# Performance work log

Hardware: AMD Instinct MI355X
Metric: run time of the kernel (lower is better)

The kernel has to match this reference:

```python
import jax, jax.numpy as jnp
import numpy as np

BS, N_AGGR, D, OUT = 4096, 4, 128, 128  # d_in per child; T is (A, D+1, D+1, OUT)


def setup_inputs() -> dict:
    key = jax.random.key(0)
    k0, k1, k2 = jax.random.split(key, 3)
    x0 = jax.random.normal(k0, (BS, N_AGGR, D), dtype=jnp.float32)
    x1 = jax.random.normal(k1, (BS, N_AGGR, D), dtype=jnp.float32)
    # xavier-uniform-style init for each T_j, stacked over the aggregator axis
    fan_in = (D + 1) * (D + 1) * OUT // (D + 1)  # torch fan heuristic scale; exact init not load-bearing
    bound = float(np.sqrt(6.0 / ((D + 1) + (D + 1) * OUT)))
    T = jax.random.uniform(k2, (N_AGGR, D + 1, D + 1, OUT), dtype=jnp.float32,
                           minval=-bound, maxval=bound)
    return {"x0": x0, "x1": x1, "T": T}


def reference(x0, x1, T):
    # x0, x1: (bs, A, D); T: (A, D+1, D+1, OUT)
    bs, A, _ = x0.shape
    ones = jnp.ones((bs, A, 1), dtype=x0.dtype)
    h0 = jnp.concatenate([x0, ones], axis=2)            # (bs, A, D+1)
    # first contraction (the per-head matmul loop, fused): (bs, A, D+1, OUT)
    r = jnp.einsum('bai,aijo->bajo', h0, T)
    h1 = jnp.concatenate([x1, ones], axis=2)            # (bs, A, D+1)
    # second contraction (the per-head bmm loop, fused): (bs, A, OUT)
    out = jnp.einsum('baj,bajo->bao', h1, r)
    return out
```

## Files before the change

kernel.cpp:

```cpp
#include <hip/hip_runtime.h>
#include <stdint.h>
#include <stddef.h>

#define NA     4
#define DDIM   128
#define OUTD   128
#define BM     256
#define BN     128
#define NTILES 261
#define TILE_B 16384
#define OUT_ELEMS (4096 * NA * OUTD)

typedef _Float16 f16;
typedef __attribute__((ext_vector_type(8)))  _Float16 f16x8;
typedef __attribute__((ext_vector_type(4)))  float    f32x4;
typedef __attribute__((ext_vector_type(16))) float    f32x16;

static const size_t TB_BYTES  = (size_t)NA * NTILES * TILE_B;
static const size_t P_BYTES   = (size_t)4 * OUT_ELEMS * sizeof(float);
static const size_t WS_NEEDED = TB_BYTES + P_BYTES;

typedef const __attribute__((address_space(1))) unsigned int guint_t;
typedef __attribute__((address_space(3))) unsigned int luint_t;

__device__ __forceinline__ void async_copy16(const void* g, void* l) {
    __builtin_amdgcn_global_load_lds((guint_t*)g, (luint_t*)l, 16, 0, 0);
}

__global__ __launch_bounds__(256) void prep_kernel(const float* __restrict__ T,
                                                   f16* __restrict__ Tb) {
    int blk  = blockIdx.x;
    int a    = blk / NTILES;
    int tile = blk - a * NTILES;
    int t    = threadIdx.x;
    f16* base = Tb + (size_t)blk * (TILE_B / 2);
    #pragma unroll
    for (int u = 0; u < 4; ++u) {
        int v   = t + u * 256;
        int w   = v >> 7;
        int col = v & 127;
        f16x8 ov;
        #pragma unroll
        for (int e = 0; e < 8; ++e) {
            int k = tile * 64 + w * 8 + e;
            int i = -1, j = 0;
            if (k < 16384)       { i = k & 127;   j = k >> 7;    }
            else if (k < 16512)  { i = 128;       j = k - 16384; }
            else if (k < 16640)  { i = k - 16512; j = 128;       }
            else if (k == 16640) { i = 128;       j = 128;       }
            float val = 0.f;
            if (i >= 0) val = T[(((size_t)a * 129 + i) * 129 + j) * 128 + col];
            ov[e] = (f16)val;
        }
        *(f16x8*)(base + (size_t)v * 8) = ov;
    }
}

template <bool ATOMIC>
__global__ __launch_bounds__(512, 2) void gemm_kernel(const float* __restrict__ x0,
                                                      const float* __restrict__ x1,
                                                      const f16* __restrict__ Tb,
                                                      float* __restrict__ dst) {
    __shared__ __align__(16) f16  h1t[128 * 256];
    __shared__ __align__(16) char Bs[3][TILE_B];

    int bid  = blockIdx.x;
    int xcd  = bid & 7, idx = bid >> 3;
    int pair = xcd * 2 + (idx >> 4);
    int mt   = idx & 15;
    int a    = pair & 3;
    int ks   = pair >> 2;

    int t    = threadIdx.x;
    int lane = t & 63, wid = t >> 6;
    int wm   = wid >> 1, wn = wid & 1;
    int l31  = lane & 31, hi = lane >> 5;
    int b0   = mt * BM;

    const char* tbb = (const char*)Tb + (size_t)a * NTILES * TILE_B;
    int nt = (ks == 0) ? 66 : 65;

    auto tile_at = [&](int tt) -> int {
        if (tt < 64) return ks * 64 + tt;
        if (ks == 0) return (tt == 64) ? 256 : 260;
        return 256 + ks;
    };
    auto stage = [&](int tt, int buf) {
        const char* src = tbb + (size_t)tile_at(tt) * TILE_B + wid * 2048 + lane * 16;
        char* dstl = &Bs[buf][wid * 2048];
        async_copy16(src,        dstl);
        async_copy16(src + 1024, dstl + 1024);
    };

    stage(0, 0);
    stage(1, 1);

    {
        int row = t & 255, hs = t >> 8;
        const float* x1r = x1 + ((size_t)(b0 + row) * NA + a) * DDIM + hs * 64;
        #pragma unroll
        for (int q = 0; q < 16; ++q) {
            f32x4 v = *(const f32x4*)(x1r + q * 4);
            #pragma unroll
            for (int e = 0; e < 4; ++e)
                h1t[(hs * 64 + q * 4 + e) * 256 + row] = (f16)v[e];
        }
    }
    f16x8 h0reg[2][8];
    #pragma unroll
    for (int fm = 0; fm < 2; ++fm) {
        int row = b0 + wm * 64 + fm * 32 + l31;
        const float* x0r = x0 + ((size_t)row * NA + a) * DDIM;
        #pragma unroll
        for (int w = 0; w < 8; ++w) {
            int wf = 2 * w + hi;
            f32x4 v0 = *(const f32x4*)(x0r + wf * 8);
            f32x4 v1 = *(const f32x4*)(x0r + wf * 8 + 4);
            f16x8 h;
            #pragma unroll
            for (int e = 0; e < 4; ++e) { h[e] = (f16)v0[e]; h[e + 4] = (f16)v1[e]; }
            h0reg[fm][w] = h;
        }
    }
    __syncthreads();

    f32x16 acc[2][2];
    #pragma unroll
    for (int i = 0; i < 2; ++i)
        #pragma unroll
        for (int j = 0; j < 2; ++j) acc[i][j] = (f32x16)0.f;

    for (int p = 0; p < 32; ++p) {
        int j = ks * 32 + p;
        f16 h1v[2];
        h1v[0] = h1t[j * 256 + (wm * 64 + l31)];
        h1v[1] = h1t[j * 256 + (wm * 64 + 32 + l31)];
        #pragma unroll
        for (int par = 0; par < 2; ++par) {
            int tt = 2 * p + par;
            asm volatile("s_waitcnt vmcnt(2)" ::: "memory");
            __builtin_amdgcn_s_barrier();
            asm volatile("" ::: "memory");
            if (tt + 2 < nt) stage(tt + 2, (tt + 2) % 3);
            const char* bb = Bs[tt % 3];
            __builtin_amdgcn_s_setprio(1);
            #pragma unroll
            for (int kk = 0; kk < 4; ++kk) {
                f16x8 bf0 = *(const f16x8*)(bb + ((kk * 2 + hi) * 128 + wn * 64 + l31) * 16);
                f16x8 bf1 = *(const f16x8*)(bb + ((kk * 2 + hi) * 128 + wn * 64 + 32 + l31) * 16);
                f16x8 a0 = h0reg[0][par * 4 + kk] * h1v[0];
                f16x8 a1 = h0reg[1][par * 4 + kk] * h1v[1];
                acc[0][0] = __builtin_amdgcn_mfma_f32_32x32x16_f16(a0, bf0, acc[0][0], 0, 0, 0);
                acc[0][1] = __builtin_amdgcn_mfma_f32_32x32x16_f16(a0, bf1, acc[0][1], 0, 0, 0);
                acc[1][0] = __builtin_amdgcn_mfma_f32_32x32x16_f16(a1, bf0, acc[1][0], 0, 0, 0);
                acc[1][1] = __builtin_amdgcn_mfma_f32_32x32x16_f16(a1, bf1, acc[1][1], 0, 0, 0);
            }
            __builtin_amdgcn_s_setprio(0);
        }
    }

    for (int tt = 64; tt < nt; ++tt) {
        int tile = tile_at(tt);
        if (tt + 1 < nt) asm volatile("s_waitcnt vmcnt(2)" ::: "memory");
        else             asm volatile("s_waitcnt vmcnt(0)" ::: "memory");
        __builtin_amdgcn_s_barrier();
        asm volatile("" ::: "memory");
        if (tt + 2 < nt) stage(tt + 2, (tt + 2) % 3);
        const char* bb = Bs[tt % 3];

        f16x8 af[2][4];
        if (tile < 258) {
            int jb = (tile - 256) * 64;
            #pragma unroll
            for (int fm = 0; fm < 2; ++fm) {
                int row = wm * 64 + fm * 32 + l31;
                #pragma unroll
                for (int kk = 0; kk < 4; ++kk) {
                    f16x8 w;
                    #pragma unroll
                    for (int e = 0; e < 8; ++e)
                        w[e] = h1t[(jb + kk * 16 + hi * 8 + e) * 256 + row];
                    af[fm][kk] = w;
                }
            }
        } else if (tile == 258) {
            #pragma unroll
            for (int fm = 0; fm < 2; ++fm)
                #pragma unroll
                for (int kk = 0; kk < 4; ++kk) af[fm][kk] = h0reg[fm][kk];
        } else if (tile == 259) {
            #pragma unroll
            for (int fm = 0; fm < 2; ++fm)
                #pragma unroll
                for (int kk = 0; kk < 4; ++kk) af[fm][kk] = h0reg[fm][4 + kk];
        } else {
            f16x8 z = (f16x8)(f16)0.f;
            f16x8 o = z;
            if (hi == 0) o[0] = (f16)1.f;
            #pragma unroll
            for (int fm = 0; fm < 2; ++fm) {
                af[fm][0] = o;
                af[fm][1] = z; af[fm][2] = z; af[fm][3] = z;
            }
        }

        __builtin_amdgcn_s_setprio(1);
        #pragma unroll
        for (int kk = 0; kk < 4; ++kk) {
            f16x8 bf0 = *(const f16x8*)(bb + ((kk * 2 + hi) * 128 + wn * 64 + l31) * 16);
            f16x8 bf1 = *(const f16x8*)(bb + ((kk * 2 + hi) * 128 + wn * 64 + 32 + l31) * 16);
            acc[0][0] = __builtin_amdgcn_mfma_f32_32x32x16_f16(af[0][kk], bf0, acc[0][0], 0, 0, 0);
            acc[0][1] = __builtin_amdgcn_mfma_f32_32x32x16_f16(af[0][kk], bf1, acc[0][1], 0, 0, 0);
            acc[1][0] = __builtin_amdgcn_mfma_f32_32x32x16_f16(af[1][kk], bf0, acc[1][0], 0, 0, 0);
            acc[1][1] = __builtin_amdgcn_mfma_f32_32x32x16_f16(af[1][kk], bf1, acc[1][1], 0, 0, 0);
        }
        __builtin_amdgcn_s_setprio(0);
    }

    float* base = ATOMIC ? dst : dst + (size_t)ks * OUT_ELEMS;
    #pragma unroll
    for (int fm = 0; fm < 2; ++fm)
        #pragma unroll
        for (int fn = 0; fn < 2; ++fn)
            #pragma unroll
            for (int r = 0; r < 16; ++r) {
                int row = b0 + wm * 64 + fm * 32 + (r & 3) + 8 * (r >> 2) + 4 * hi;
                int col = wn * 64 + fn * 32 + l31;
                size_t off = ((size_t)row * NA + a) * OUTD + col;
                if (ATOMIC) unsafeAtomicAdd(&base[off], acc[fm][fn][r]);
                else        base[off] = acc[fm][fn][r];
            }
}

__global__ __launch_bounds__(256) void reduce_kernel(const float* __restrict__ P,
                                                     float* __restrict__ out) {
    int i = blockIdx.x * 256 + threadIdx.x;
    f32x4 s = ((const f32x4*)P)[i];
    s += ((const f32x4*)(P + OUT_ELEMS))[i];
    s += ((const f32x4*)(P + 2 * (size_t)OUT_ELEMS))[i];
    s += ((const f32x4*)(P + 3 * (size_t)OUT_ELEMS))[i];
    ((f32x4*)out)[i] = s;
}

__global__ __launch_bounds__(128) void fallback_kernel(const float* __restrict__ x0,
                                                       const float* __restrict__ x1,
                                                       const float* __restrict__ T,
                                                       float* __restrict__ out) {
    int ba = blockIdx.x;
    int b = ba >> 2, a = ba & 3;
    int o = threadIdx.x;
    const float* h0 = x0 + ((size_t)b * NA + a) * DDIM;
    const float* h1 = x1 + ((size_t)b * NA + a) * DDIM;
    float acc = 0.f;
    for (int i = 0; i < 129; ++i) {
        float h0i = (i < 128) ? h0[i] : 1.f;
        const float* Trow = T + (((size_t)a * 129 + i) * 129) * 128 + o;
        float part = 0.f;
        for (int j = 0; j < 129; ++j) {
            float h1j = (j < 128) ? h1[j] : 1.f;
            part += h1j * Trow[(size_t)j * 128];
        }
        acc += h0i * part;
    }
    out[((size_t)b * NA + a) * OUTD + o] = acc;
}

extern "C" void kernel_launch(void* const* d_in, const int* in_sizes, int n_in,
                              void* d_out, int out_size, void* d_ws, size_t ws_size,
                              hipStream_t stream) {
    const float* x0 = (const float*)d_in[0];
    const float* x1 = (const float*)d_in[1];
    const float* T  = (const float*)d_in[2];
    float* out = (float*)d_out;

    if (ws_size < TB_BYTES) {
        fallback_kernel<<<4096 * NA, 128, 0, stream>>>(x0, x1, T, out);
        return;
    }

    f16* Tb = (f16*)d_ws;
    prep_kernel<<<NA * NTILES, 256, 0, stream>>>(T, Tb);

    if (ws_size >= WS_NEEDED) {
        float* P = (float*)((char*)d_ws + TB_BYTES);
        gemm_kernel<false><<<256, 512, 0, stream>>>(x0, x1, Tb, P);
        reduce_kernel<<<OUT_ELEMS / 4 / 256, 256, 0, stream>>>(P, out);
    } else {
        hipMemsetAsync(d_out, 0, (size_t)out_size * sizeof(float), stream);
        gemm_kernel<true><<<256, 512, 0, stream>>>(x0, x1, Tb, out);
    }
}
```

Baseline: 105.4 us.

## Reshape warp tiles to 128x32 and halve the h1 LDS buffer

```diff
diff --git a/kernel.cpp b/kernel.cpp
--- a/kernel.cpp
+++ b/kernel.cpp
@@ -61,7 +61,7 @@
                                                       const float* __restrict__ x1,
                                                       const f16* __restrict__ Tb,
                                                       float* __restrict__ dst) {
-    __shared__ __align__(16) f16  h1t[128 * 256];
+    __shared__ __align__(16) f16  h1t[64 * 256];
     __shared__ __align__(16) char Bs[3][TILE_B];
 
     int bid  = blockIdx.x;
@@ -73,17 +73,21 @@
 
     int t    = threadIdx.x;
     int lane = t & 63, wid = t >> 6;
-    int wm   = wid >> 1, wn = wid & 1;
+    int wm   = wid >> 2, wn = wid & 3;
     int l31  = lane & 31, hi = lane >> 5;
     int b0   = mt * BM;
 
     const char* tbb = (const char*)Tb + (size_t)a * NTILES * TILE_B;
-    int nt = (ks == 0) ? 66 : 65;
+    int nt    = (ks == 1) ? 66 : 65;
+    int jbase = ks * 32;
+    int jn    = (ks == 0 || ks == 2) ? 64 : 32;
 
     auto tile_at = [&](int tt) -> int {
         if (tt < 64) return ks * 64 + tt;
-        if (ks == 0) return (tt == 64) ? 256 : 260;
-        return 256 + ks;
+        if (ks == 0) return 256;
+        if (ks == 1) return (tt == 64) ? 258 : 260;
+        if (ks == 2) return 257;
+        return 259;
     };
     auto stage = [&](int tt, int buf) {
         const char* src = tbb + (size_t)tile_at(tt) * TILE_B + wid * 2048 + lane * 16;
@@ -97,19 +101,19 @@
 
     {
         int row = t & 255, hs = t >> 8;
-        const float* x1r = x1 + ((size_t)(b0 + row) * NA + a) * DDIM + hs * 64;
-        #pragma unroll
-        for (int q = 0; q < 16; ++q) {
+        const float* x1r = x1 + ((size_t)(b0 + row) * NA + a) * DDIM + jbase;
+        int half = jn >> 1;
+        for (int q = hs * (half >> 2); q < (hs + 1) * (half >> 2); ++q) {
             f32x4 v = *(const f32x4*)(x1r + q * 4);
             #pragma unroll
             for (int e = 0; e < 4; ++e)
-                h1t[(hs * 64 + q * 4 + e) * 256 + row] = (f16)v[e];
-        }
-    }
-    f16x8 h0reg[2][8];
-    #pragma unroll
-    for (int fm = 0; fm < 2; ++fm) {
-        int row = b0 + wm * 64 + fm * 32 + l31;
+                h1t[(q * 4 + e) * 256 + row] = (f16)v[e];
+        }
+    }
+    f16x8 h0reg[4][8];
+    #pragma unroll
+    for (int fm = 0; fm < 4; ++fm) {
+        int row = b0 + wm * 128 + fm * 32 + l31;
         const float* x0r = x0 + ((size_t)row * NA + a) * DDIM;
         #pragma unroll
         for (int w = 0; w < 8; ++w) {
@@ -124,17 +128,15 @@
     }
     __syncthreads();
 
-    f32x16 acc[2][2];
-    #pragma unroll
-    for (int i = 0; i < 2; ++i)
-        #pragma unroll
-        for (int j = 0; j < 2; ++j) acc[i][j] = (f32x16)0.f;
+    f32x16 acc[4];
+    #pragma unroll
+    for (int i = 0; i < 4; ++i) acc[i] = (f32x16)0.f;
 
     for (int p = 0; p < 32; ++p) {
-        int j = ks * 32 + p;
-        f16 h1v[2];
-        h1v[0] = h1t[j * 256 + (wm * 64 + l31)];
-        h1v[1] = h1t[j * 256 + (wm * 64 + 32 + l31)];
+        f16 h1v[4];
+        #pragma unroll
+        for (int fm = 0; fm < 4; ++fm)
+            h1v[fm] = h1t[p * 256 + (wm * 128 + fm * 32 + l31)];
         #pragma unroll
         for (int par = 0; par < 2; ++par) {
             int tt = 2 * p + par;
@@ -146,90 +148,64 @@
             __builtin_amdgcn_s_setprio(1);
             #pragma unroll
             for (int kk = 0; kk < 4; ++kk) {
-                f16x8 bf0 = *(const f16x8*)(bb + ((kk * 2 + hi) * 128 + wn * 64 + l31) * 16);
-                f16x8 bf1 = *(const f16x8*)(bb + ((kk * 2 + hi) * 128 + wn * 64 + 32 + l31) * 16);
-                f16x8 a0 = h0reg[0][par * 4 + kk] * h1v[0];
-                f16x8 a1 = h0reg[1][par * 4 + kk] * h1v[1];
-                acc[0][0] = __builtin_amdgcn_mfma_f32_32x32x16_f16(a0, bf0, acc[0][0], 0, 0, 0);
-                acc[0][1] = __builtin_amdgcn_mfma_f32_32x32x16_f16(a0, bf1, acc[0][1], 0, 0, 0);
-                acc[1][0] = __builtin_amdgcn_mfma_f32_32x32x16_f16(a1, bf0, acc[1][0], 0, 0, 0);
-                acc[1][1] = __builtin_amdgcn_mfma_f32_32x32x16_f16(a1, bf1, acc[1][1], 0, 0, 0);
+                f16x8 bf = *(const f16x8*)(bb + ((kk * 2 + hi) * 128 + wn * 32 + l31) * 16);
+                #pragma unroll
+                for (int fm = 0; fm < 4; ++fm) {
+                    f16x8 af = h0reg[fm][par * 4 + kk] * h1v[fm];
+                    acc[fm] = __builtin_amdgcn_mfma_f32_32x32x16_f16(af, bf, acc[fm], 0, 0, 0);
+                }
             }
             __builtin_amdgcn_s_setprio(0);
         }
     }
 
     for (int tt = 64; tt < nt; ++tt) {
-        int tile = tile_at(tt);
         if (tt + 1 < nt) asm volatile("s_waitcnt vmcnt(2)" ::: "memory");
         else             asm volatile("s_waitcnt vmcnt(0)" ::: "memory");
         __builtin_amdgcn_s_barrier();
         asm volatile("" ::: "memory");
-        if (tt + 2 < nt) stage(tt + 2, (tt + 2) % 3);
         const char* bb = Bs[tt % 3];
-
-        f16x8 af[2][4];
-        if (tile < 258) {
-            int jb = (tile - 256) * 64;
-            #pragma unroll
-            for (int fm = 0; fm < 2; ++fm) {
-                int row = wm * 64 + fm * 32 + l31;
-                #pragma unroll
-                for (int kk = 0; kk < 4; ++kk) {
-                    f16x8 w;
+        bool icorr_lo = (ks == 1) && (tt == 64);
+        bool onehot   = (ks == 1) && (tt == 65);
+
+        __builtin_amdgcn_s_setprio(1);
+        #pragma unroll
+        for (int kk = 0; kk < 4; ++kk) {
+            f16x8 bf = *(const f16x8*)(bb + ((kk * 2 + hi) * 128 + wn * 32 + l31) * 16);
+            #pragma unroll
+            for (int fm = 0; fm < 4; ++fm) {
+                f16x8 af;
+                if (ks == 0 || ks == 2) {
+                    int row = wm * 128 + fm * 32 + l31;
                     #pragma unroll
                     for (int e = 0; e < 8; ++e)
-                        w[e] = h1t[(jb + kk * 16 + hi * 8 + e) * 256 + row];
-                    af[fm][kk] = w;
+                        af[e] = h1t[(kk * 16 + hi * 8 + e) * 256 + row];
+                } else if (ks == 3) {
+                    af = h0reg[fm][4 + kk];
+                } else if (icorr_lo) {
+                    af = h0reg[fm][kk];
+                } else {
+                    af = (f16x8)(f16)0.f;
+                    if (kk == 0 && hi == 0) af[0] = (f16)1.f;
                 }
+                (void)onehot;
+                acc[fm] = __builtin_amdgcn_mfma_f32_32x32x16_f16(af, bf, acc[fm], 0, 0, 0);
             }
-        } else if (tile == 258) {
-            #pragma unroll
-            for (int fm = 0; fm < 2; ++fm)
-                #pragma unroll
-                for (int kk = 0; kk < 4; ++kk) af[fm][kk] = h0reg[fm][kk];
-        } else if (tile == 259) {
-            #pragma unroll
-            for (int fm = 0; fm < 2; ++fm)
-                #pragma unroll
-                for (int kk = 0; kk < 4; ++kk) af[fm][kk] = h0reg[fm][4 + kk];
-        } else {
-            f16x8 z = (f16x8)(f16)0.f;
-            f16x8 o = z;
-            if (hi == 0) o[0] = (f16)1.f;
-            #pragma unroll
-            for (int fm = 0; fm < 2; ++fm) {
-                af[fm][0] = o;
-                af[fm][1] = z; af[fm][2] = z; af[fm][3] = z;
-            }
-        }
-
-        __builtin_amdgcn_s_setprio(1);
-        #pragma unroll
-        for (int kk = 0; kk < 4; ++kk) {
-            f16x8 bf0 = *(const f16x8*)(bb + ((kk * 2 + hi) * 128 + wn * 64 + l31) * 16);
-            f16x8 bf1 = *(const f16x8*)(bb + ((kk * 2 + hi) * 128 + wn * 64 + 32 + l31) * 16);
-            acc[0][0] = __builtin_amdgcn_mfma_f32_32x32x16_f16(af[0][kk], bf0, acc[0][0], 0, 0, 0);
-            acc[0][1] = __builtin_amdgcn_mfma_f32_32x32x16_f16(af[0][kk], bf1, acc[0][1], 0, 0, 0);
-            acc[1][0] = __builtin_amdgcn_mfma_f32_32x32x16_f16(af[1][kk], bf0, acc[1][0], 0, 0, 0);
-            acc[1][1] = __builtin_amdgcn_mfma_f32_32x32x16_f16(af[1][kk], bf1, acc[1][1], 0, 0, 0);
         }
         __builtin_amdgcn_s_setprio(0);
     }
 
     float* base = ATOMIC ? dst : dst + (size_t)ks * OUT_ELEMS;
     #pragma unroll
-    for (int fm = 0; fm < 2; ++fm)
-        #pragma unroll
-        for (int fn = 0; fn < 2; ++fn)
-            #pragma unroll
-            for (int r = 0; r < 16; ++r) {
-                int row = b0 + wm * 64 + fm * 32 + (r & 3) + 8 * (r >> 2) + 4 * hi;
-                int col = wn * 64 + fn * 32 + l31;
-                size_t off = ((size_t)row * NA + a) * OUTD + col;
-                if (ATOMIC) unsafeAtomicAdd(&base[off], acc[fm][fn][r]);
-                else        base[off] = acc[fm][fn][r];
-            }
+    for (int fm = 0; fm < 4; ++fm)
+        #pragma unroll
+        for (int r = 0; r < 16; ++r) {
+            int row = b0 + wm * 128 + fm * 32 + (r & 3) + 8 * (r >> 2) + 4 * hi;
+            int col = wn * 32 + l31;
+            size_t off = ((size_t)row * NA + a) * OUTD + col;
+            if (ATOMIC) unsafeAtomicAdd(&base[off], acc[fm][r]);
+            else        base[off] = acc[fm][r];
+        }
 }
 
 __global__ __launch_bounds__(256) void reduce_kernel(const float* __restrict__ P,
```

Result: slower. 114.1 us (+8.3%).
